# Performance work log

Hardware: AMD Instinct MI355X
Metric: run time of the kernel (lower is better)

The kernel has to match this reference:

```python
import jax, jax.numpy as jnp
import numpy as np

B, S, H, STEPS = 4096, 169, 64, 24  # batch, input seq (window 168 + covariate row), hidden, rollout steps


def _lstm(xseq, Wih, Whh, bih, bhh, h0, c0):
    """PyTorch-style single-layer LSTM. xseq: [B,T,D] -> ([B,T,H], hT, cT). Gate order i,f,g,o."""
    xg = jnp.einsum('btd,gd->btg', xseq, Wih) + (bih + bhh)  # precompute input proj [B,T,4H]

    def step(carry, xg_t):
        h, c = carry
        g = xg_t + h @ Whh.T
        i, f, gg, o = jnp.split(g, 4, axis=-1)
        c = jax.nn.sigmoid(f) * c + jax.nn.sigmoid(i) * jnp.tanh(gg)
        h = jax.nn.sigmoid(o) * jnp.tanh(c)
        return (h, c), h

    (hT, cT), hs = jax.lax.scan(step, (h0, c0), jnp.swapaxes(xg, 0, 1))
    return jnp.swapaxes(hs, 0, 1), hT, cT


def reference(x, Wih1, Whh1, bih1, bhh1, Wih2, Whh2, bih2, bhh2, fc1_w, fc1_b, fc2_w, fc2_b):
    win, d = x[:, :-1, :], x[:, -1, :]  # [B,168,1], [B,1]
    z = jnp.zeros((x.shape[0], H), x.dtype)

    def outer(win, _):
        h1s, h1, c1 = _lstm(win, Wih1, Whh1, bih1, bhh1, z, z)
        h1s = jax.nn.relu(h1s)
        # lstm2 is seeded with lstm1's final (h, c) state, as in the torch code
        h2s, _, _ = _lstm(h1s, Wih2, Whh2, bih2, bhh2, h1, c1)
        feat = jnp.concatenate([jax.nn.relu(h2s[:, -1, :]), d], axis=1)  # [B,65]
        out = (feat @ fc1_w.T + fc1_b) @ fc2_w.T + fc2_b  # [B,1] (no relu between fc1/fc2)
        win = jnp.concatenate([win[:, 1:, :], out[:, :, None]], axis=1)  # slide window
        return win, out[:, 0]

    _, outs = jax.lax.scan(outer, win, None, length=STEPS)  # outs: [24,B]
    return jnp.swapaxes(outs, 0, 1)  # [B,24]


def setup_inputs() -> dict:
    key = jax.random.key(0)
    ks = jax.random.split(key, 14)
    bnd = 1.0 / np.sqrt(H)

    def u(k, shape):
        return jax.random.uniform(k, shape, jnp.float32, -bnd, bnd)

    return {
        'x': jax.random.normal(ks[0], (B, S, 1), jnp.float32),
        'Wih1': u(ks[1], (4 * H, 1)),
        'Whh1': u(ks[2], (4 * H, H)),
        'bih1': u(ks[3], (4 * H,)),
        'bhh1': u(ks[4], (4 * H,)),
        'Wih2': u(ks[5], (4 * H, H)),
        'Whh2': u(ks[6], (4 * H, H)),
        'bih2': u(ks[7], (4 * H,)),
        'bhh2': u(ks[8], (4 * H,)),
        'fc1_w': u(ks[9], (64, 65)),
        'fc1_b': u(ks[10], (64,)),
        'fc2_w': u(ks[11], (1, 64)),
        'fc2_b': u(ks[12], (1,)),
    }
```

## Files before the change

kernel.cpp:

```cpp
#include <hip/hip_runtime.h>
#include <stdint.h>

#define NB 16
#define WIN 168
#define NSTEPS 24
#define NBLK (4096/NB)
#define NT 512

typedef __attribute__((ext_vector_type(8))) short bf16x8;
typedef __attribute__((ext_vector_type(4))) float f32x4;

#if __has_builtin(__builtin_amdgcn_rcpf)
#define RCPF(x) __builtin_amdgcn_rcpf(x)
#else
#define RCPF(x) (1.0f / (x))
#endif
#if __has_builtin(__builtin_amdgcn_exp2f)
#define EXP2F(x) __builtin_amdgcn_exp2f(x)
#else
#define EXP2F(x) __expf((x) * 0.6931471805599453f)
#endif

__device__ __forceinline__ float sigm(float x){
  return RCPF(1.0f + EXP2F(x * -1.4426950408889634f));
}
__device__ __forceinline__ float sigtanh(float a, float b){
  float A = EXP2F(a * -1.4426950408889634f);
  float B = EXP2F(fabsf(b) * -2.8853900817779268f);
  float t = (1.0f - B) * RCPF((1.0f + A) * (1.0f + B));
  uint32_t sb = __builtin_bit_cast(uint32_t, b) & 0x80000000u;
  return __builtin_bit_cast(float, __builtin_bit_cast(uint32_t, t) ^ sb);
}

__device__ __forceinline__ uint32_t bf_rn(float f){
  uint32_t u = __builtin_bit_cast(uint32_t, f);
  return (u + 0x7FFFu + ((u >> 16) & 1u)) >> 16;
}
__device__ __forceinline__ float bf_f(uint32_t s){
  return __builtin_bit_cast(float, s << 16);
}
__device__ __forceinline__ void split_t(float f, uint32_t& hi, uint32_t& lo){
  uint32_t u = __builtin_bit_cast(uint32_t, f);
  hi = u >> 16;
  lo = bf_rn(f - bf_f(hi));
}
__device__ __forceinline__ void split_s(float f, short& hi, short& lo){
  uint32_t h = bf_rn(f);
  hi = (short)h;
  lo = (short)bf_rn(f - bf_f(h));
}
__device__ __forceinline__ f32x4 mfma16(bf16x8 a, bf16x8 b, f32x4 c){
  return __builtin_amdgcn_mfma_f32_16x16x32_bf16(a, b, c, 0, 0, 0);
}

__device__ __forceinline__ void lstm_epi(const f32x4 acc[4], float c[4], float hn[4]){
  #pragma unroll
  for (int r = 0; r < 4; r++){
    float cn = __builtin_fmaf(sigm(acc[1][r]), c[r], sigtanh(acc[0][r], acc[2][r]));
    c[r] = cn;
    hn[r] = sigtanh(acc[3][r], cn);
  }
}

#define FROW 136
#define FBLK 544
#define FB(buf,hl,kt) ((((buf)*2 + (hl))*2 + (kt)) * FBLK)
#define BUF_INTS (2*FBLK)

__global__ __launch_bounds__(NT, 2) void lstm_fused_kernel(
  const float* __restrict__ x,    const float* __restrict__ Wih1, const float* __restrict__ Whh1,
  const float* __restrict__ bih1, const float* __restrict__ bhh1,
  const float* __restrict__ Wih2, const float* __restrict__ Whh2,
  const float* __restrict__ bih2, const float* __restrict__ bhh2,
  const float* __restrict__ fc1w, const float* __restrict__ fc1b,
  const float* __restrict__ fc2w, const float* __restrict__ fc2b,
  float* __restrict__ out, short* __restrict__ hist)
{
  __shared__ __align__(16) short aS[2*2*2*FBLK];
  __shared__ __align__(16) short bS[2*2*2*FBLK];
  __shared__ float cS[64][16];
  __shared__ float win_s[WIN][NB];
  __shared__ float Hlast[NB][68];
  __shared__ float fc1w_s[64*68];
  __shared__ float dval_s[NB];

  const int tid = threadIdx.x;
  const int wv8 = tid >> 6;
  const int wv  = wv8 & 3;
  const bool isA = (wv8 < 4);
  const int ln  = tid & 63;
  const int q   = ln >> 4;
  const int n   = ln & 15;
  const int bg0 = blockIdx.x * NB;
  const int u0  = 16*wv + 4*q;
  const int kt_  = u0 >> 5;
  const int q2_  = (u0 >> 3) & 3;
  const int jj0_ = u0 & 7;
  const int rdo  = q*FROW + n*8;
  const int wro  = q2_*FROW + n*8 + jj0_;
  const int gwo  = kt_*512 + q2_*128 + n*8 + jj0_;
  const int ro   = q*128 + n*8;
  short* __restrict__ hblk = hist + (size_t)blockIdx.x * WIN * 2048;

  for (int i = tid; i < WIN*NB; i += NT){ int t = i >> 4, b = i & 15; win_s[t][b] = x[(bg0 + b)*169 + t]; }
  for (int i = tid; i < 64*65; i += NT){ int j = i / 65, k = i % 65; fc1w_s[j*68 + k] = fc1w[i]; }
  if (tid < NB) dval_s[tid] = x[(bg0 + tid)*169 + 168];

  const float fc1b_r = fc1b[ln];
  const float fc2w_r = fc2w[ln];
  const float fc2b_r = fc2b[0];

  auto fc_head = [&](int s){
    float o2[2];
    #pragma unroll
    for (int bi = 0; bi < 2; bi++){
      const int b = 2*wv8 + bi;
      float a1 = fc1b_r;
      #pragma unroll
      for (int k4 = 0; k4 < 16; k4++){
        const float* wp = &fc1w_s[ln*68 + k4*4];
        const float* hp = &Hlast[b][k4*4];
        a1 += wp[0]*hp[0] + wp[1]*hp[1] + wp[2]*hp[2] + wp[3]*hp[3];
      }
      a1 += dval_s[b] * fc1w_s[ln*68 + 64];
      float v = a1 * fc2w_r;
      #pragma unroll
      for (int off = 32; off > 0; off >>= 1) v += __shfl_xor(v, off);
      o2[bi] = v + fc2b_r;
    }
    if (ln == 0){
      #pragma unroll
      for (int bi = 0; bi < 2; bi++){
        const int b = 2*wv8 + bi;
        out[(bg0 + b)*24 + s] = o2[bi];
        win_s[s % WIN][b] = o2[bi];
      }
    }
  };

  if (isA){
    bf16x8 A1hi[4][2], A1lo[4][2], Ain1[4];
    f32x4 b1c[4];
    #pragma unroll
    for (int e = 0; e < 4; e++){
      const int ja = 64*e + 16*wv + n;
      #pragma unroll
      for (int kt = 0; kt < 2; kt++){
        const float* pw = Whh1 + ja*64 + kt*32 + q*8;
        #pragma unroll
        for (int jj = 0; jj < 8; jj++){ short h,l; split_s(pw[jj], h, l); A1hi[e][kt][jj] = h; A1lo[e][kt][jj] = l; }
      }
      bf16x8 ain = {0,0,0,0,0,0,0,0};
      if (q == 0){ short wh, wl; split_s(Wih1[ja], wh, wl); ain[0] = wh; ain[1] = wh; ain[2] = wl; }
      Ain1[e] = ain;
      const int jc = 64*e + u0;
      #pragma unroll
      for (int r = 0; r < 4; r++) b1c[e][r] = bih1[jc+r] + bhh1[jc+r];
    }
    float c1[4];

    auto lstm1 = [&](int rb, int wb, int slot, int t, bool first){
      f32x4 acc[4];
      bf16x8 bin = {0,0,0,0,0,0,0,0};
      { float xv = win_s[slot][n]; uint32_t xh, xl; split_t(xv, xh, xl);
        if (q == 0){ bin[0] = (short)xh; bin[1] = (short)xl; bin[2] = (short)xh; } }
      if (first){
        #pragma unroll
        for (int e = 0; e < 4; e++) acc[e] = mfma16(Ain1[e], bin, b1c[e]);
      } else {
        bf16x8 Bh0 = *(const bf16x8*)&aS[FB(rb,0,0)+rdo];
        bf16x8 Bl0 = *(const bf16x8*)&aS[FB(rb,1,0)+rdo];
        bf16x8 Bh1 = *(const bf16x8*)&aS[FB(rb,0,1)+rdo];
        bf16x8 Bl1 = *(const bf16x8*)&aS[FB(rb,1,1)+rdo];
        #pragma unroll
        for (int e = 0; e < 4; e++){
          f32x4 a = b1c[e];
          a = mfma16(A1hi[e][0], Bh0, a);
          a = mfma16(A1hi[e][0], Bl0, a);
          a = mfma16(A1lo[e][0], Bh0, a);
          a = mfma16(A1hi[e][1], Bh1, a);
          a = mfma16(A1hi[e][1], Bl1, a);
          a = mfma16(A1lo[e][1], Bh1, a);
          a = mfma16(Ain1[e], bin, a);
          acc[e] = a;
        }
      }
      float hn[4];
      lstm_epi(acc, c1, hn);
      uint32_t ph[4], pl[4];
      #pragma unroll
      for (int r = 0; r < 4; r++) split_t(hn[r], ph[r], pl[r]);
      *(uint2*)&aS[FB(wb,0,kt_)+wro] = make_uint2(ph[0] | (ph[1]<<16), ph[2] | (ph[3]<<16));
      *(uint2*)&aS[FB(wb,1,kt_)+wro] = make_uint2(pl[0] | (pl[1]<<16), pl[2] | (pl[3]<<16));
      uint32_t sh[4], sl[4];
      #pragma unroll
      for (int r = 0; r < 4; r++){ bool pos = hn[r] > 0.0f; sh[r] = pos ? ph[r] : 0u; sl[r] = pos ? pl[r] : 0u; }
      short* Hp = hblk + (size_t)t * 2048;
      *(uint2*)&Hp[gwo]        = make_uint2(sh[0] | (sh[1]<<16), sh[2] | (sh[3]<<16));
      *(uint2*)&Hp[1024 + gwo] = make_uint2(sl[0] | (sl[1]<<16), sl[2] | (sl[3]<<16));
    };

    #pragma unroll
    for (int r = 0; r < 4; r++) c1[r] = 0.0f;
    for (int t = 0; t < WIN; t++){
      __syncthreads();
      lstm1(t & 1, (t & 1) ^ 1, t, t, t == 0);
    }
    #pragma unroll
    for (int r = 0; r < 4; r++) cS[u0 + r][n] = c1[r];

    for (int sg = 1; sg < NSTEPS; sg++){
      #pragma unroll
      for (int r = 0; r < 4; r++) c1[r] = 0.0f;
      int slot = sg;
      __syncthreads();
      lstm1(0, 1, slot, 0, true);
      slot++;
      for (int t = 1; t < WIN-1; t++){
        __syncthreads();
        lstm1(t & 1, (t & 1) ^ 1, slot, t, false);
        slot++; if (slot == WIN) slot = 0;
      }
      __syncthreads();
      __syncthreads();
      fc_head(sg - 1);
      __syncthreads();
      lstm1(1, 0, slot, WIN-1, false);
      #pragma unroll
      for (int r = 0; r < 4; r++) cS[u0 + r][n] = c1[r];
    }

    for (int i = 0; i < WIN + 1; i++) __syncthreads();
    fc_head(NSTEPS - 1);

  } else {
    bf16x8 A2hi[4][4], A2lo[4][4];
    f32x4 b2c[4];
    #pragma unroll
    for (int e = 0; e < 4; e++){
      const int ja = 64*e + 16*wv + n;
      #pragma unroll
      for (int kt = 0; kt < 4; kt++){
        const float* pw = (kt < 2 ? (Wih2 + ja*64 + kt*32) : (Whh2 + ja*64 + (kt-2)*32)) + q*8;
        #pragma unroll
        for (int jj = 0; jj < 8; jj++){ short h,l; split_s(pw[jj], h, l); A2hi[e][kt][jj] = h; A2lo[e][kt][jj] = l; }
      }
      const int jc = 64*e + u0;
      #pragma unroll
      for (int r = 0; r < 4; r++) b2c[e][r] = bih2[jc+r] + bhh2[jc+r];
    }
    float c2[4];
    bf16x8 ch0, cl0, ch1, cl1, nh0, nl0, nh1, nl1;

    auto loadc = [&](int t){
      const short* Hp = hblk + (size_t)t * 2048;
      ch0 = *(const bf16x8*)&Hp[ro];
      cl0 = *(const bf16x8*)&Hp[1024 + ro];
      ch1 = *(const bf16x8*)&Hp[512 + ro];
      cl1 = *(const bf16x8*)&Hp[1536 + ro];
    };
    auto loadn = [&](int t){
      const short* Hp = hblk + (size_t)t * 2048;
      nh0 = *(const bf16x8*)&Hp[ro];
      nl0 = *(const bf16x8*)&Hp[1024 + ro];
      nh1 = *(const bf16x8*)&Hp[512 + ro];
      nl1 = *(const bf16x8*)&Hp[1536 + ro];
    };
    auto shift = [&](){ ch0 = nh0; cl0 = nl0; ch1 = nh1; cl1 = nl1; };

    auto lstm2 = [&](const short* Sr, int rb, short* Sw, int wb, bool last){
      bf16x8 L2h0 = *(const bf16x8*)&Sr[FB(rb,0,0)+rdo];
      bf16x8 L2l0 = *(const bf16x8*)&Sr[FB(rb,1,0)+rdo];
      bf16x8 L2h1 = *(const bf16x8*)&Sr[FB(rb,0,1)+rdo];
      bf16x8 L2l1 = *(const bf16x8*)&Sr[FB(rb,1,1)+rdo];
      f32x4 acc[4];
      #pragma unroll
      for (int e = 0; e < 4; e++){
        f32x4 a = b2c[e];
        a = mfma16(A2hi[e][0], ch0, a);
        a = mfma16(A2hi[e][0], cl0, a);
        a = mfma16(A2lo[e][0], ch0, a);
        a = mfma16(A2hi[e][1], ch1, a);
        a = mfma16(A2hi[e][1], cl1, a);
        a = mfma16(A2lo[e][1], ch1, a);
        a = mfma16(A2hi[e][2], L2h0, a);
        a = mfma16(A2hi[e][2], L2l0, a);
        a = mfma16(A2lo[e][2], L2h0, a);
        a = mfma16(A2hi[e][3], L2h1, a);
        a = mfma16(A2hi[e][3], L2l1, a);
        a = mfma16(A2lo[e][3], L2h1, a);
        acc[e] = a;
      }
      float hn[4];
      lstm_epi(acc, c2, hn);
      if (!last){
        uint32_t ph[4], pl[4];
        #pragma unroll
        for (int r = 0; r < 4; r++) split_t(hn[r], ph[r], pl[r]);
        *(uint2*)&Sw[FB(wb,0,kt_)+wro] = make_uint2(ph[0] | (ph[1]<<16), ph[2] | (ph[3]<<16));
        *(uint2*)&Sw[FB(wb,1,kt_)+wro] = make_uint2(pl[0] | (pl[1]<<16), pl[2] | (pl[3]<<16));
      } else {
        #pragma unroll
        for (int r = 0; r < 4; r++) Hlast[n][u0 + r] = fmaxf(hn[r], 0.0f);
      }
    };

    for (int i = 0; i < WIN; i++) __syncthreads();

    for (int sg = 1; sg < NSTEPS; sg++){
      loadc(0);
      loadn(1);
      __syncthreads();
      #pragma unroll
      for (int r = 0; r < 4; r++) c2[r] = cS[u0 + r][n];
      lstm2(aS, 0, bS, 1, false);
      shift();
      for (int t = 1; t < WIN-1; t++){
        __syncthreads();
        loadn(t + 1);
        lstm2(bS, t & 1, bS, (t & 1) ^ 1, false);
        shift();
      }
      __syncthreads();
      lstm2(bS, 1, bS, 0, true);
      __syncthreads();
      fc_head(sg - 1);
      __syncthreads();
    }

    {
      loadc(0);
      loadn(1);
      __syncthreads();
      #pragma unroll
      for (int r = 0; r < 4; r++) c2[r] = cS[u0 + r][n];
      lstm2(aS, 0, bS, 1, false);
      shift();
      for (int t = 1; t < WIN-1; t++){
        __syncthreads();
        loadn(t + 1);
        lstm2(bS, t & 1, bS, (t & 1) ^ 1, false);
        shift();
      }
      __syncthreads();
      lstm2(bS, 1, bS, 0, true);
      __syncthreads();
      fc_head(NSTEPS - 1);
    }
  }
}

__global__ __launch_bounds__(256, 1) void lstm_fallback_kernel(
  const float* __restrict__ x,    const float* __restrict__ Wih1, const float* __restrict__ Whh1,
  const float* __restrict__ bih1, const float* __restrict__ bhh1,
  const float* __restrict__ Wih2, const float* __restrict__ Whh2,
  const float* __restrict__ bih2, const float* __restrict__ bhh2,
  const float* __restrict__ fc1w, const float* __restrict__ fc1b,
  const float* __restrict__ fc2w, const float* __restrict__ fc2b,
  float* __restrict__ out)
{
  __shared__ __align__(16) short aS[2*2*2*FBLK];
  __shared__ __align__(16) short r1f[2*2*2*FBLK];
  __shared__ __align__(16) short rlf[2*2*2*FBLK];
  __shared__ float win_s[WIN][NB];
  __shared__ float Hlast[NB][68];
  __shared__ float fc1w_s[64*68];
  __shared__ float dval_s[NB];

  const int tid = threadIdx.x;
  const int wv  = tid >> 6;
  const int ln  = tid & 63;
  const int q   = ln >> 4;
  const int n   = ln & 15;
  const int bg0 = blockIdx.x * NB;
  const int u0  = 16*wv + 4*q;
  const int kt_  = u0 >> 5;
  const int q2_  = (u0 >> 3) & 3;
  const int jj0_ = u0 & 7;
  const int rdo  = q*FROW + n*8;
  const int wro  = q2_*FROW + n*8 + jj0_;

  for (int i = tid; i < WIN*NB; i += 256){ int t = i >> 4, b = i & 15; win_s[t][b] = x[(bg0 + b)*169 + t]; }
  for (int i = tid; i < 64*65; i += 256){ int j = i / 65, k = i % 65; fc1w_s[j*68 + k] = fc1w[i]; }
  if (tid < NB) dval_s[tid] = x[(bg0 + tid)*169 + 168];

  const float fc1b_r = fc1b[ln];
  const float fc2w_r = fc2w[ln];
  const float fc2b_r = fc2b[0];

  bf16x8 A1hi[4][2], A1lo[4][2], Ain1[4];
  bf16x8 A2hi[4][4], A2lo[4][4];
  f32x4 b1c[4], b2c[4];
  #pragma unroll
  for (int e = 0; e < 4; e++){
    const int ja = 64*e + 16*wv + n;
    #pragma unroll
    for (int kt = 0; kt < 2; kt++){
      const float* pw = Whh1 + ja*64 + kt*32 + q*8;
      #pragma unroll
      for (int jj = 0; jj < 8; jj++){ short h,l; split_s(pw[jj], h, l); A1hi[e][kt][jj] = h; A1lo[e][kt][jj] = l; }
    }
    #pragma unroll
    for (int kt = 0; kt < 4; kt++){
      const float* pw = (kt < 2 ? (Wih2 + ja*64 + kt*32) : (Whh2 + ja*64 + (kt-2)*32)) + q*8;
      #pragma unroll
      for (int jj = 0; jj < 8; jj++){ short h,l; split_s(pw[jj], h, l); A2hi[e][kt][jj] = h; A2lo[e][kt][jj] = l; }
    }
    bf16x8 ain = {0,0,0,0,0,0,0,0};
    if (q == 0){ short wh, wl; split_s(Wih1[ja], wh, wl); ain[0] = wh; ain[1] = wh; ain[2] = wl; }
    Ain1[e] = ain;
    const int jc = 64*e + u0;
    #pragma unroll
    for (int r = 0; r < 4; r++){
      b1c[e][r] = bih1[jc+r] + bhh1[jc+r];
      b2c[e][r] = bih2[jc+r] + bhh2[jc+r];
    }
  }

  float c1[4], c2[4], c1r[4];

  auto lstm1_step = [&](short* S, float* cst, int rb, int wb, int slot, bool relu_out){
    bf16x8 Bh0 = *(const bf16x8*)&S[FB(rb,0,0)+rdo];
    bf16x8 Bl0 = *(const bf16x8*)&S[FB(rb,1,0)+rdo];
    bf16x8 Bh1 = *(const bf16x8*)&S[FB(rb,0,1)+rdo];
    bf16x8 Bl1 = *(const bf16x8*)&S[FB(rb,1,1)+rdo];
    bf16x8 bin = {0,0,0,0,0,0,0,0};
    { float xv = win_s[slot][n]; uint32_t xh, xl; split_t(xv, xh, xl);
      if (q == 0){ bin[0] = (short)xh; bin[1] = (short)xl; bin[2] = (short)xh; } }
    f32x4 acc[4];
    #pragma unroll
    for (int e = 0; e < 4; e++){
      f32x4 a = b1c[e];
      a = mfma16(A1hi[e][0], Bh0, a);
      a = mfma16(A1hi[e][0], Bl0, a);
      a = mfma16(A1lo[e][0], Bh0, a);
      a = mfma16(A1hi[e][1], Bh1, a);
      a = mfma16(A1hi[e][1], Bl1, a);
      a = mfma16(A1lo[e][1], Bh1, a);
      a = mfma16(Ain1[e], bin, a);
      acc[e] = a;
    }
    float hn[4];
    lstm_epi(acc, cst, hn);
    uint32_t ph[4], pl[4];
    #pragma unroll
    for (int r = 0; r < 4; r++) split_t(hn[r], ph[r], pl[r]);
    *(uint2*)&S[FB(wb,0,kt_)+wro] = make_uint2(ph[0] | (ph[1]<<16), ph[2] | (ph[3]<<16));
    *(uint2*)&S[FB(wb,1,kt_)+wro] = make_uint2(pl[0] | (pl[1]<<16), pl[2] | (pl[3]<<16));
    if (relu_out){
      uint32_t sh[4], sl[4];
      #pragma unroll
      for (int r = 0; r < 4; r++){ bool pos = hn[r] > 0.0f; sh[r] = pos ? ph[r] : 0u; sl[r] = pos ? pl[r] : 0u; }
      *(uint2*)&rlf[FB(rb,0,kt_)+wro] = make_uint2(sh[0] | (sh[1]<<16), sh[2] | (sh[3]<<16));
      *(uint2*)&rlf[FB(rb,1,kt_)+wro] = make_uint2(sl[0] | (sl[1]<<16), sl[2] | (sl[3]<<16));
    }
  };

  auto lstm2_core = [&](bf16x8 L1h0, bf16x8 L1l0, bf16x8 L1h1, bf16x8 L1l1,
                        int rbuf, int wbuf, bool last){
    bf16x8 L2h0 = *(const bf16x8*)&aS[FB(rbuf,0,0)+rdo];
    bf16x8 L2l0 = *(const bf16x8*)&aS[FB(rbuf,1,0)+rdo];
    bf16x8 L2h1 = *(const bf16x8*)&aS[FB(rbuf,0,1)+rdo];
    bf16x8 L2l1 = *(const bf16x8*)&aS[FB(rbuf,1,1)+rdo];
    f32x4 acc[4];
    #pragma unroll
    for (int e = 0; e < 4; e++){
      f32x4 a = b2c[e];
      a = mfma16(A2hi[e][0], L1h0, a);
      a = mfma16(A2hi[e][0], L1l0, a);
      a = mfma16(A2lo[e][0], L1h0, a);
      a = mfma16(A2hi[e][1], L1h1, a);
      a = mfma16(A2hi[e][1], L1l1, a);
      a = mfma16(A2lo[e][1], L1h1, a);
      a = mfma16(A2hi[e][2], L2h0, a);
      a = mfma16(A2hi[e][2], L2l0, a);
      a = mfma16(A2lo[e][2], L2h0, a);
      a = mfma16(A2hi[e][3], L2h1, a);
      a = mfma16(A2hi[e][3], L2l1, a);
      a = mfma16(A2lo[e][3], L2h1, a);
      acc[e] = a;
    }
    float hn[4];
    lstm_epi(acc, c2, hn);
    if (!last){
      uint32_t ph[4], pl[4];
      #pragma unroll
      for (int r = 0; r < 4; r++) split_t(hn[r], ph[r], pl[r]);
      *(uint2*)&aS[FB(wbuf,0,kt_)+wro] = make_uint2(ph[0] | (ph[1]<<16), ph[2] | (ph[3]<<16));
      *(uint2*)&aS[FB(wbuf,1,kt_)+wro] = make_uint2(pl[0] | (pl[1]<<16), pl[2] | (pl[3]<<16));
    } else {
      #pragma unroll
      for (int r = 0; r < 4; r++) Hlast[n][u0 + r] = fmaxf(hn[r], 0.0f);
    }
  };

  for (int s = 0; s < NSTEPS; s++){
    { int* p = (int*)&aS[0];
      for (int i = tid; i < BUF_INTS; i += 256) p[i] = 0; }
    #pragma unroll
    for (int r = 0; r < 4; r++) c1[r] = 0.0f;
    int slot = s;
    for (int t = 0; t < WIN; t++){
      __syncthreads();
      lstm1_step(aS, c1, t & 1, (t & 1) ^ 1, slot, false);
      slot++; if (slot == WIN) slot = 0;
    }
    #pragma unroll
    for (int r = 0; r < 4; r++){ c2[r] = c1[r]; c1r[r] = 0.0f; }
    { int* p = (int*)&r1f[0];
      for (int i = tid; i < BUF_INTS; i += 256) p[i] = 0; }
    slot = s;
    __syncthreads();
    lstm1_step(r1f, c1r, 0, 1, slot, true);
    slot++;
    for (int i = 1; i < WIN; i++){
      __syncthreads();
      const int rb = i & 1, wb = rb ^ 1;
      lstm1_step(r1f, c1r, rb, wb, slot, true);
      bf16x8 L1h0 = *(const bf16x8*)&rlf[FB(wb,0,0)+rdo];
      bf16x8 L1l0 = *(const bf16x8*)&rlf[FB(wb,1,0)+rdo];
      bf16x8 L1h1 = *(const bf16x8*)&rlf[FB(wb,0,1)+rdo];
      bf16x8 L1l1 = *(const bf16x8*)&rlf[FB(wb,1,1)+rdo];
      lstm2_core(L1h0, L1l0, L1h1, L1l1, wb, rb, false);
      slot++; if (slot == WIN) slot = 0;
    }
    __syncthreads();
    {
      const int rb = (WIN - 1) & 1;
      bf16x8 L1h0 = *(const bf16x8*)&rlf[FB(rb,0,0)+rdo];
      bf16x8 L1l0 = *(const bf16x8*)&rlf[FB(rb,1,0)+rdo];
      bf16x8 L1h1 = *(const bf16x8*)&rlf[FB(rb,0,1)+rdo];
      bf16x8 L1l1 = *(const bf16x8*)&rlf[FB(rb,1,1)+rdo];
      lstm2_core(L1h0, L1l0, L1h1, L1l1, rb, 0, true);
    }
    __syncthreads();
    {
      float o4[4];
      #pragma unroll
      for (int bi = 0; bi < 4; bi++){
        const int b = 4*wv + bi;
        float a1 = fc1b_r;
        #pragma unroll
        for (int k4 = 0; k4 < 16; k4++){
          const float* wp = &fc1w_s[ln*68 + k4*4];
          const float* hp = &Hlast[b][k4*4];
          a1 += wp[0]*hp[0] + wp[1]*hp[1] + wp[2]*hp[2] + wp[3]*hp[3];
        }
        a1 += dval_s[b] * fc1w_s[ln*68 + 64];
        float v = a1 * fc2w_r;
        #pragma unroll
        for (int off = 32; off > 0; off >>= 1) v += __shfl_xor(v, off);
        o4[bi] = v + fc2b_r;
      }
      if (ln == 0){
        #pragma unroll
        for (int bi = 0; bi < 4; bi++){
          const int b = 4*wv + bi;
          out[(bg0 + b)*24 + s] = o4[bi];
          win_s[s % WIN][b] = o4[bi];
        }
      }
    }
  }
}

extern "C" void kernel_launch(void* const* d_in, const int* in_sizes, int n_in,
                              void* d_out, int out_size, void* d_ws, size_t ws_size,
                              hipStream_t stream) {
  (void)in_sizes; (void)n_in; (void)out_size;
  const size_t need = (size_t)NBLK * WIN * 2048 * sizeof(short);
  if (ws_size >= need){
    lstm_fused_kernel<<<dim3(NBLK), dim3(NT), 0, stream>>>(
        (const float*)d_in[0], (const float*)d_in[1], (const float*)d_in[2],
        (const float*)d_in[3], (const float*)d_in[4], (const float*)d_in[5],
        (const float*)d_in[6], (const float*)d_in[7], (const float*)d_in[8],
        (const float*)d_in[9], (const float*)d_in[10], (const float*)d_in[11],
        (const float*)d_in[12], (float*)d_out, (short*)d_ws);
  } else {
    lstm_fallback_kernel<<<dim3(NBLK), dim3(256), 0, stream>>>(
        (const float*)d_in[0], (const float*)d_in[1], (const float*)d_in[2],
        (const float*)d_in[3], (const float*)d_in[4], (const float*)d_in[5],
        (const float*)d_in[6], (const float*)d_in[7], (const float*)d_in[8],
        (const float*)d_in[9], (const float*)d_in[10], (const float*)d_in[11],
        (const float*)d_in[12], (float*)d_out);
  }
}
```

Measured before the change: 4.958 ms.

## Replace block-wide barriers with LDS counter flags between LSTM1 and LSTM2 warp groups

Replaces the per-timestep __syncthreads between the LSTM1 and LSTM2 wave groups with LDS atomic counters and spin-waits, so each group waits only on the progress it actually depends on. The FC head moves entirely into the LSTM2 waves. The aim is to let the two layers run in a looser pipeline and drop full-block barrier stalls. It adds spin-wait polling, relies on volatile LDS reads and manual waitcnt fences for memory ordering, and carries a risk of subtle races or hangs.

Result: slower. 5.931 ms (+19.6%).

```diff
diff --git a/kernel.cpp b/kernel.cpp
--- a/kernel.cpp
+++ b/kernel.cpp
@@ -5,7 +5,6 @@
 #define WIN 168
 #define NSTEPS 24
 #define NBLK (4096/NB)
-#define NT 512
 
 typedef __attribute__((ext_vector_type(8))) short bf16x8;
 typedef __attribute__((ext_vector_type(4))) float f32x4;
@@ -67,7 +66,11 @@
 #define FB(buf,hl,kt) ((((buf)*2 + (hl))*2 + (kt)) * FBLK)
 #define BUF_INTS (2*FBLK)
 
-__global__ __launch_bounds__(NT, 2) void lstm_fused_kernel(
+#define LGKM_FENCE() __asm__ volatile("s_waitcnt lgkmcnt(0)" ::: "memory")
+#define VM_FENCE()   __asm__ volatile("s_waitcnt vmcnt(0)" ::: "memory")
+#define CC_FENCE()   __asm__ volatile("" ::: "memory")
+
+__global__ __launch_bounds__(512, 2) void lstm_decoupled_kernel(
   const float* __restrict__ x,    const float* __restrict__ Wih1, const float* __restrict__ Whh1,
   const float* __restrict__ bih1, const float* __restrict__ bhh1,
   const float* __restrict__ Wih2, const float* __restrict__ Whh2,
@@ -83,6 +86,7 @@
   __shared__ float Hlast[NB][68];
   __shared__ float fc1w_s[64*68];
   __shared__ float dval_s[NB];
+  __shared__ int barA, barB;
 
   const int tid = threadIdx.x;
   const int wv8 = tid >> 6;
@@ -102,41 +106,19 @@
   const int ro   = q*128 + n*8;
   short* __restrict__ hblk = hist + (size_t)blockIdx.x * WIN * 2048;
 
-  for (int i = tid; i < WIN*NB; i += NT){ int t = i >> 4, b = i & 15; win_s[t][b] = x[(bg0 + b)*169 + t]; }
-  for (int i = tid; i < 64*65; i += NT){ int j = i / 65, k = i % 65; fc1w_s[j*68 + k] = fc1w[i]; }
+  for (int i = tid; i < WIN*NB; i += 512){ int t = i >> 4, b = i & 15; win_s[t][b] = x[(bg0 + b)*169 + t]; }
+  for (int i = tid; i < 64*65; i += 512){ int j = i / 65, k = i % 65; fc1w_s[j*68 + k] = fc1w[i]; }
   if (tid < NB) dval_s[tid] = x[(bg0 + tid)*169 + 168];
+  if (tid == 0){ barA = 0; barB = 0; }
 
   const float fc1b_r = fc1b[ln];
   const float fc2w_r = fc2w[ln];
   const float fc2b_r = fc2b[0];
 
-  auto fc_head = [&](int s){
-    float o2[2];
-    #pragma unroll
-    for (int bi = 0; bi < 2; bi++){
-      const int b = 2*wv8 + bi;
-      float a1 = fc1b_r;
-      #pragma unroll
-      for (int k4 = 0; k4 < 16; k4++){
-        const float* wp = &fc1w_s[ln*68 + k4*4];
-        const float* hp = &Hlast[b][k4*4];
-        a1 += wp[0]*hp[0] + wp[1]*hp[1] + wp[2]*hp[2] + wp[3]*hp[3];
-      }
-      a1 += dval_s[b] * fc1w_s[ln*68 + 64];
-      float v = a1 * fc2w_r;
-      #pragma unroll
-      for (int off = 32; off > 0; off >>= 1) v += __shfl_xor(v, off);
-      o2[bi] = v + fc2b_r;
-    }
-    if (ln == 0){
-      #pragma unroll
-      for (int bi = 0; bi < 2; bi++){
-        const int b = 2*wv8 + bi;
-        out[(bg0 + b)*24 + s] = o2[bi];
-        win_s[s % WIN][b] = o2[bi];
-      }
-    }
-  };
+  __syncthreads();
+
+  volatile int* vA = &barA;
+  volatile int* vB = &barB;
 
   if (isA){
     bf16x8 A1hi[4][2], A1lo[4][2], Ain1[4];
@@ -158,80 +140,73 @@
       for (int r = 0; r < 4; r++) b1c[e][r] = bih1[jc+r] + bhh1[jc+r];
     }
     float c1[4];
-
-    auto lstm1 = [&](int rb, int wb, int slot, int t, bool first){
-      f32x4 acc[4];
-      bf16x8 bin = {0,0,0,0,0,0,0,0};
-      { float xv = win_s[slot][n]; uint32_t xh, xl; split_t(xv, xh, xl);
-        if (q == 0){ bin[0] = (short)xh; bin[1] = (short)xl; bin[2] = (short)xh; } }
-      if (first){
-        #pragma unroll
-        for (int e = 0; e < 4; e++) acc[e] = mfma16(Ain1[e], bin, b1c[e]);
-      } else {
-        bf16x8 Bh0 = *(const bf16x8*)&aS[FB(rb,0,0)+rdo];
-        bf16x8 Bl0 = *(const bf16x8*)&aS[FB(rb,1,0)+rdo];
-        bf16x8 Bh1 = *(const bf16x8*)&aS[FB(rb,0,1)+rdo];
-        bf16x8 Bl1 = *(const bf16x8*)&aS[FB(rb,1,1)+rdo];
-        #pragma unroll
-        for (int e = 0; e < 4; e++){
-          f32x4 a = b1c[e];
-          a = mfma16(A1hi[e][0], Bh0, a);
-          a = mfma16(A1hi[e][0], Bl0, a);
-          a = mfma16(A1lo[e][0], Bh0, a);
-          a = mfma16(A1hi[e][1], Bh1, a);
-          a = mfma16(A1hi[e][1], Bl1, a);
-          a = mfma16(A1lo[e][1], Bh1, a);
-          a = mfma16(Ain1[e], bin, a);
-          acc[e] = a;
-        }
-      }
-      float hn[4];
-      lstm_epi(acc, c1, hn);
-      uint32_t ph[4], pl[4];
-      #pragma unroll
-      for (int r = 0; r < 4; r++) split_t(hn[r], ph[r], pl[r]);
-      *(uint2*)&aS[FB(wb,0,kt_)+wro] = make_uint2(ph[0] | (ph[1]<<16), ph[2] | (ph[3]<<16));
-      *(uint2*)&aS[FB(wb,1,kt_)+wro] = make_uint2(pl[0] | (pl[1]<<16), pl[2] | (pl[3]<<16));
-      uint32_t sh[4], sl[4];
-      #pragma unroll
-      for (int r = 0; r < 4; r++){ bool pos = hn[r] > 0.0f; sh[r] = pos ? ph[r] : 0u; sl[r] = pos ? pl[r] : 0u; }
-      short* Hp = hblk + (size_t)t * 2048;
-      *(uint2*)&Hp[gwo]        = make_uint2(sh[0] | (sh[1]<<16), sh[2] | (sh[3]<<16));
-      *(uint2*)&Hp[1024 + gwo] = make_uint2(sl[0] | (sl[1]<<16), sl[2] | (sl[3]<<16));
-    };
-
-    #pragma unroll
-    for (int r = 0; r < 4; r++) c1[r] = 0.0f;
-    for (int t = 0; t < WIN; t++){
-      __syncthreads();
-      lstm1(t & 1, (t & 1) ^ 1, t, t, t == 0);
-    }
-    #pragma unroll
-    for (int r = 0; r < 4; r++) cS[u0 + r][n] = c1[r];
-
-    for (int sg = 1; sg < NSTEPS; sg++){
+    int gA = 0;
+
+    for (int sg = 0; sg < NSTEPS; sg++){
       #pragma unroll
       for (int r = 0; r < 4; r++) c1[r] = 0.0f;
       int slot = sg;
-      __syncthreads();
-      lstm1(0, 1, slot, 0, true);
-      slot++;
-      for (int t = 1; t < WIN-1; t++){
-        __syncthreads();
-        lstm1(t & 1, (t & 1) ^ 1, slot, t, false);
+      for (int t = 0; t < WIN; t++){
+        int tb = 0;
+        if (sg > 0) tb = (t == WIN-1) ? 4*169*sg : 4*((sg-1)*169 + t + 1);
+        if (ln == 0){
+          const int ta = 4*gA;
+          while (*vA < ta) {}
+          while (*vB < tb) {}
+        }
+        CC_FENCE();
+        {
+          const int rb = t & 1, wb = rb ^ 1;
+          f32x4 acc[4];
+          bf16x8 bin = {0,0,0,0,0,0,0,0};
+          { float xv = win_s[slot][n]; uint32_t xh, xl; split_t(xv, xh, xl);
+            if (q == 0){ bin[0] = (short)xh; bin[1] = (short)xl; bin[2] = (short)xh; } }
+          if (t == 0){
+            #pragma unroll
+            for (int e = 0; e < 4; e++) acc[e] = mfma16(Ain1[e], bin, b1c[e]);
+          } else {
+            bf16x8 Bh0 = *(const bf16x8*)&aS[FB(rb,0,0)+rdo];
+            bf16x8 Bl0 = *(const bf16x8*)&aS[FB(rb,1,0)+rdo];
+            bf16x8 Bh1 = *(const bf16x8*)&aS[FB(rb,0,1)+rdo];
+            bf16x8 Bl1 = *(const bf16x8*)&aS[FB(rb,1,1)+rdo];
+            #pragma unroll
+            for (int e = 0; e < 4; e++){
+              f32x4 a = b1c[e];
+              a = mfma16(A1hi[e][0], Bh0, a);
+              a = mfma16(A1hi[e][0], Bl0, a);
+              a = mfma16(A1lo[e][0], Bh0, a);
+              a = mfma16(A1hi[e][1], Bh1, a);
+              a = mfma16(A1hi[e][1], Bl1, a);
+              a = mfma16(A1lo[e][1], Bh1, a);
+              a = mfma16(Ain1[e], bin, a);
+              acc[e] = a;
+            }
+          }
+          float hn[4];
+          lstm_epi(acc, c1, hn);
+          uint32_t ph[4], pl[4];
+          #pragma unroll
+          for (int r = 0; r < 4; r++) split_t(hn[r], ph[r], pl[r]);
+          *(uint2*)&aS[FB(wb,0,kt_)+wro] = make_uint2(ph[0] | (ph[1]<<16), ph[2] | (ph[3]<<16));
+          *(uint2*)&aS[FB(wb,1,kt_)+wro] = make_uint2(pl[0] | (pl[1]<<16), pl[2] | (pl[3]<<16));
+          uint32_t sh[4], sl[4];
+          #pragma unroll
+          for (int r = 0; r < 4; r++){ bool pos = hn[r] > 0.0f; sh[r] = pos ? ph[r] : 0u; sl[r] = pos ? pl[r] : 0u; }
+          short* Hp = hblk + (size_t)t * 2048;
+          *(uint2*)&Hp[gwo]        = make_uint2(sh[0] | (sh[1]<<16), sh[2] | (sh[3]<<16));
+          *(uint2*)&Hp[1024 + gwo] = make_uint2(sl[0] | (sl[1]<<16), sl[2] | (sl[3]<<16));
+          if (t == WIN-1){
+            #pragma unroll
+            for (int r = 0; r < 4; r++) cS[u0 + r][n] = c1[r];
+          }
+        }
+        LGKM_FENCE();
+        if (t == WIN-1) VM_FENCE();
+        if (ln == 0) atomicAdd(&barA, 1);
+        gA++;
         slot++; if (slot == WIN) slot = 0;
       }
-      __syncthreads();
-      __syncthreads();
-      fc_head(sg - 1);
-      __syncthreads();
-      lstm1(1, 0, slot, WIN-1, false);
-      #pragma unroll
-      for (int r = 0; r < 4; r++) cS[u0 + r][n] = c1[r];
-    }
-
-    for (int i = 0; i < WIN + 1; i++) __syncthreads();
-    fc_head(NSTEPS - 1);
+    }
 
   } else {
     bf16x8 A2hi[4][4], A2lo[4][4];
@@ -251,14 +226,8 @@
     }
     float c2[4];
     bf16x8 ch0, cl0, ch1, cl1, nh0, nl0, nh1, nl1;
-
-    auto loadc = [&](int t){
-      const short* Hp = hblk + (size_t)t * 2048;
-      ch0 = *(const bf16x8*)&Hp[ro];
-      cl0 = *(const bf16x8*)&Hp[1024 + ro];
-      ch1 = *(const bf16x8*)&Hp[512 + ro];
-      cl1 = *(const bf16x8*)&Hp[1536 + ro];
-    };
+    int gB = 0;
+
     auto loadn = [&](int t){
       const short* Hp = hblk + (size_t)t * 2048;
       nh0 = *(const bf16x8*)&Hp[ro];
@@ -266,86 +235,104 @@
       nh1 = *(const bf16x8*)&Hp[512 + ro];
       nl1 = *(const bf16x8*)&Hp[1536 + ro];
     };
-    auto shift = [&](){ ch0 = nh0; cl0 = nl0; ch1 = nh1; cl1 = nl1; };
-
-    auto lstm2 = [&](const short* Sr, int rb, short* Sw, int wb, bool last){
-      bf16x8 L2h0 = *(const bf16x8*)&Sr[FB(rb,0,0)+rdo];
-      bf16x8 L2l0 = *(const bf16x8*)&Sr[FB(rb,1,0)+rdo];
-      bf16x8 L2h1 = *(const bf16x8*)&Sr[FB(rb,0,1)+rdo];
-      bf16x8 L2l1 = *(const bf16x8*)&Sr[FB(rb,1,1)+rdo];
-      f32x4 acc[4];
-      #pragma unroll
-      for (int e = 0; e < 4; e++){
-        f32x4 a = b2c[e];
-        a = mfma16(A2hi[e][0], ch0, a);
-        a = mfma16(A2hi[e][0], cl0, a);
-        a = mfma16(A2lo[e][0], ch0, a);
-        a = mfma16(A2hi[e][1], ch1, a);
-        a = mfma16(A2hi[e][1], cl1, a);
-        a = mfma16(A2lo[e][1], ch1, a);
-        a = mfma16(A2hi[e][2], L2h0, a);
-        a = mfma16(A2hi[e][2], L2l0, a);
-        a = mfma16(A2lo[e][2], L2h0, a);
-        a = mfma16(A2hi[e][3], L2h1, a);
-        a = mfma16(A2hi[e][3], L2l1, a);
-        a = mfma16(A2lo[e][3], L2h1, a);
-        acc[e] = a;
-      }
-      float hn[4];
-      lstm_epi(acc, c2, hn);
-      if (!last){
-        uint32_t ph[4], pl[4];
+
+    for (int sb = 0; sb < NSTEPS; sb++){
+      for (int t = 0; t < WIN; t++){
+        if (ln == 0){
+          const int tb = 4*gB;
+          while (*vB < tb) {}
+          if (t == 0){ const int ta = 4*168*(sb+1); while (*vA < ta) {} }
+        }
+        CC_FENCE();
+        if (t == 0){
+          #pragma unroll
+          for (int r = 0; r < 4; r++) c2[r] = cS[u0 + r][n];
+          const short* Hp = hblk;
+          ch0 = *(const bf16x8*)&Hp[ro];
+          cl0 = *(const bf16x8*)&Hp[1024 + ro];
+          ch1 = *(const bf16x8*)&Hp[512 + ro];
+          cl1 = *(const bf16x8*)&Hp[1536 + ro];
+          loadn(1);
+        } else if (t < WIN-1){
+          loadn(t + 1);
+        }
+        {
+          const bool last = (t == WIN-1);
+          const short* Sr = (t == 0) ? aS : bS;
+          const int rb = (t == 0) ? 0 : (t & 1);
+          const int wb = (t == 0) ? 1 : ((t & 1) ^ 1);
+          bf16x8 L2h0 = *(const bf16x8*)&Sr[FB(rb,0,0)+rdo];
+          bf16x8 L2l0 = *(const bf16x8*)&Sr[FB(rb,1,0)+rdo];
+          bf16x8 L2h1 = *(const bf16x8*)&Sr[FB(rb,0,1)+rdo];
+          bf16x8 L2l1 = *(const bf16x8*)&Sr[FB(rb,1,1)+rdo];
+          f32x4 acc[4];
+          #pragma unroll
+          for (int e = 0; e < 4; e++){
+            f32x4 a = b2c[e];
+            a = mfma16(A2hi[e][0], ch0, a);
+            a = mfma16(A2hi[e][0], cl0, a);
+            a = mfma16(A2lo[e][0], ch0, a);
+            a = mfma16(A2hi[e][1], ch1, a);
+            a = mfma16(A2hi[e][1], cl1, a);
+            a = mfma16(A2lo[e][1], ch1, a);
+            a = mfma16(A2hi[e][2], L2h0, a);
+            a = mfma16(A2hi[e][2], L2l0, a);
+            a = mfma16(A2lo[e][2], L2h0, a);
+            a = mfma16(A2hi[e][3], L2h1, a);
+            a = mfma16(A2hi[e][3], L2l1, a);
+            a = mfma16(A2lo[e][3], L2h1, a);
+            acc[e] = a;
+          }
+          float hn[4];
+          lstm_epi(acc, c2, hn);
+          if (!last){
+            uint32_t ph[4], pl[4];
+            #pragma unroll
+            for (int r = 0; r < 4; r++) split_t(hn[r], ph[r], pl[r]);
+            *(uint2*)&bS[FB(wb,0,kt_)+wro] = make_uint2(ph[0] | (ph[1]<<16), ph[2] | (ph[3]<<16));
+            *(uint2*)&bS[FB(wb,1,kt_)+wro] = make_uint2(pl[0] | (pl[1]<<16), pl[2] | (pl[3]<<16));
+          } else {
+            #pragma unroll
+            for (int r = 0; r < 4; r++) Hlast[n][u0 + r] = fmaxf(hn[r], 0.0f);
+          }
+          ch0 = nh0; cl0 = nl0; ch1 = nh1; cl1 = nl1;
+        }
+        LGKM_FENCE();
+        if (ln == 0) atomicAdd(&barB, 1);
+        gB++;
+      }
+      if (ln == 0){ const int tb = 4*gB; while (*vB < tb) {} }
+      CC_FENCE();
+      {
+        float o4[4];
         #pragma unroll
-        for (int r = 0; r < 4; r++) split_t(hn[r], ph[r], pl[r]);
-        *(uint2*)&Sw[FB(wb,0,kt_)+wro] = make_uint2(ph[0] | (ph[1]<<16), ph[2] | (ph[3]<<16));
-        *(uint2*)&Sw[FB(wb,1,kt_)+wro] = make_uint2(pl[0] | (pl[1]<<16), pl[2] | (pl[3]<<16));
-      } else {
-        #pragma unroll
-        for (int r = 0; r < 4; r++) Hlast[n][u0 + r] = fmaxf(hn[r], 0.0f);
-      }
-    };
-
-    for (int i = 0; i < WIN; i++) __syncthreads();
-
-    for (int sg = 1; sg < NSTEPS; sg++){
-      loadc(0);
-      loadn(1);
-      __syncthreads();
-      #pragma unroll
-      for (int r = 0; r < 4; r++) c2[r] = cS[u0 + r][n];
-      lstm2(aS, 0, bS, 1, false);
-      shift();
-      for (int t = 1; t < WIN-1; t++){
-        __syncthreads();
-        loadn(t + 1);
-        lstm2(bS, t & 1, bS, (t & 1) ^ 1, false);
-        shift();
-      }
-      __syncthreads();
-      lstm2(bS, 1, bS, 0, true);
-      __syncthreads();
-      fc_head(sg - 1);
-      __syncthreads();
-    }
-
-    {
-      loadc(0);
-      loadn(1);
-      __syncthreads();
-      #pragma unroll
-      for (int r = 0; r < 4; r++) c2[r] = cS[u0 + r][n];
-      lstm2(aS, 0, bS, 1, false);
-      shift();
-      for (int t = 1; t < WIN-1; t++){
-        __syncthreads();
-        loadn(t + 1);
-        lstm2(bS, t & 1, bS, (t & 1) ^ 1, false);
-        shift();
-      }
-      __syncthreads();
-      lstm2(bS, 1, bS, 0, true);
-      __syncthreads();
-      fc_head(NSTEPS - 1);
+        for (int bi = 0; bi < 4; bi++){
+          const int b = 4*wv + bi;
+          float a1 = fc1b_r;
+          #pragma unroll
+          for (int k4 = 0; k4 < 16; k4++){
+            const float* wp = &fc1w_s[ln*68 + k4*4];
+            const float* hp = &Hlast[b][k4*4];
+            a1 += wp[0]*hp[0] + wp[1]*hp[1] + wp[2]*hp[2] + wp[3]*hp[3];
+          }
+          a1 += dval_s[b] * fc1w_s[ln*68 + 64];
+          float v = a1 * fc2w_r;
+          #pragma unroll
+          for (int off = 32; off > 0; off >>= 1) v += __shfl_xor(v, off);
+          o4[bi] = v + fc2b_r;
+        }
+        if (ln == 0){
+          #pragma unroll
+          for (int bi = 0; bi < 4; bi++){
+            const int b = 4*wv + bi;
+            out[(bg0 + b)*24 + sb] = o4[bi];
+            win_s[sb][b] = o4[bi];
+          }
+        }
+      }
+      LGKM_FENCE();
+      if (ln == 0) atomicAdd(&barB, 1);
+      gB++;
     }
   }
 }
@@ -570,7 +557,7 @@
   (void)in_sizes; (void)n_in; (void)out_size;
   const size_t need = (size_t)NBLK * WIN * 2048 * sizeof(short);
   if (ws_size >= need){
-    lstm_fused_kernel<<<dim3(NBLK), dim3(NT), 0, stream>>>(
+    lstm_decoupled_kernel<<<dim3(NBLK), dim3(512), 0, stream>>>(
         (const float*)d_in[0], (const float*)d_in[1], (const float*)d_in[2],
         (const float*)d_in[3], (const float*)d_in[4], (const float*)d_in[5],
         (const float*)d_in[6], (const float*)d_in[7], (const float*)d_in[8],
```

## Move LSTM2 input projection to LSTM1 warps via shared-memory partial sums

Applied to the files above, without the earlier changes.

The input-projection half of LSTM2's gate GEMM (Wih2·relu(h1)) moves from the LSTM2 warps to the LSTM1 warps. The LSTM1 warps now load the h1 history and compute that partial, then write it to a double-buffered shared array. LSTM2 warps start from these partials, so each of their steps runs only the recurrent Whh2 half, halving MFMA work on the LSTM2 critical path. In exchange the LSTM1 warps carry more registers and MFMA work, and shared-memory use grows by about 32 KB, which may limit the two-blocks-per-CU occupancy.

New measurement: 5.224 ms. 5.4% more time.

```diff
diff --git a/kernel.cpp b/kernel.cpp
--- a/kernel.cpp
+++ b/kernel.cpp
@@ -66,6 +66,10 @@
 #define FBLK 544
 #define FB(buf,hl,kt) ((((buf)*2 + (hl))*2 + (kt)) * FBLK)
 #define BUF_INTS (2*FBLK)
+
+#define PS_E   256
+#define PS_WV  (4*PS_E)
+#define PS_PB  (4*PS_WV)
 
 __global__ __launch_bounds__(NT, 2) void lstm_fused_kernel(
   const float* __restrict__ x,    const float* __restrict__ Wih1, const float* __restrict__ Whh1,
@@ -78,6 +82,7 @@
 {
   __shared__ __align__(16) short aS[2*2*2*FBLK];
   __shared__ __align__(16) short bS[2*2*2*FBLK];
+  __shared__ __align__(16) float pS[2*PS_PB];
   __shared__ float cS[64][16];
   __shared__ float win_s[WIN][NB];
   __shared__ float Hlast[NB][68];
@@ -100,6 +105,7 @@
   const int wro  = q2_*FROW + n*8 + jj0_;
   const int gwo  = kt_*512 + q2_*128 + n*8 + jj0_;
   const int ro   = q*128 + n*8;
+  const int pso  = wv*PS_WV + q*64 + n*4;
   short* __restrict__ hblk = hist + (size_t)blockIdx.x * WIN * 2048;
 
   for (int i = tid; i < WIN*NB; i += NT){ int t = i >> 4, b = i & 15; win_s[t][b] = x[(bg0 + b)*169 + t]; }
@@ -140,7 +146,8 @@
 
   if (isA){
     bf16x8 A1hi[4][2], A1lo[4][2], Ain1[4];
-    f32x4 b1c[4];
+    bf16x8 A2hi[4][2], A2lo[4][2];
+    f32x4 b1c[4], b2c[4];
     #pragma unroll
     for (int e = 0; e < 4; e++){
       const int ja = 64*e + 16*wv + n;
@@ -149,15 +156,46 @@
         const float* pw = Whh1 + ja*64 + kt*32 + q*8;
         #pragma unroll
         for (int jj = 0; jj < 8; jj++){ short h,l; split_s(pw[jj], h, l); A1hi[e][kt][jj] = h; A1lo[e][kt][jj] = l; }
+      }
+      #pragma unroll
+      for (int kt = 0; kt < 2; kt++){
+        const float* pw = Wih2 + ja*64 + kt*32 + q*8;
+        #pragma unroll
+        for (int jj = 0; jj < 8; jj++){ short h,l; split_s(pw[jj], h, l); A2hi[e][kt][jj] = h; A2lo[e][kt][jj] = l; }
       }
       bf16x8 ain = {0,0,0,0,0,0,0,0};
       if (q == 0){ short wh, wl; split_s(Wih1[ja], wh, wl); ain[0] = wh; ain[1] = wh; ain[2] = wl; }
       Ain1[e] = ain;
       const int jc = 64*e + u0;
       #pragma unroll
-      for (int r = 0; r < 4; r++) b1c[e][r] = bih1[jc+r] + bhh1[jc+r];
+      for (int r = 0; r < 4; r++){
+        b1c[e][r] = bih1[jc+r] + bhh1[jc+r];
+        b2c[e][r] = bih2[jc+r] + bhh2[jc+r];
+      }
     }
     float c1[4];
+    bf16x8 rh0, rl0, rh1, rl1;
+
+    auto hloadA = [&](int t){
+      const short* Hp = hblk + (size_t)t * 2048;
+      rh0 = *(const bf16x8*)&Hp[ro];
+      rl0 = *(const bf16x8*)&Hp[1024 + ro];
+      rh1 = *(const bf16x8*)&Hp[512 + ro];
+      rl1 = *(const bf16x8*)&Hp[1536 + ro];
+    };
+    auto partial2 = [&](int pb){
+      #pragma unroll
+      for (int e = 0; e < 4; e++){
+        f32x4 a = b2c[e];
+        a = mfma16(A2hi[e][0], rh0, a);
+        a = mfma16(A2hi[e][0], rl0, a);
+        a = mfma16(A2lo[e][0], rh0, a);
+        a = mfma16(A2hi[e][1], rh1, a);
+        a = mfma16(A2hi[e][1], rl1, a);
+        a = mfma16(A2lo[e][1], rh1, a);
+        *(f32x4*)&pS[pb*PS_PB + pso + e*PS_E] = a;
+      }
+    };
 
     auto lstm1 = [&](int rb, int wb, int slot, int t, bool first){
       f32x4 acc[4];
@@ -202,10 +240,14 @@
 
     #pragma unroll
     for (int r = 0; r < 4; r++) c1[r] = 0.0f;
-    for (int t = 0; t < WIN; t++){
+    for (int t = 0; t < WIN-1; t++){
       __syncthreads();
       lstm1(t & 1, (t & 1) ^ 1, t, t, t == 0);
     }
+    __syncthreads();
+    hloadA(0);
+    lstm1(1, 0, WIN-1, WIN-1, false);
+    partial2(0);
     #pragma unroll
     for (int r = 0; r < 4; r++) cS[u0 + r][n] = c1[r];
 
@@ -214,81 +256,68 @@
       for (int r = 0; r < 4; r++) c1[r] = 0.0f;
       int slot = sg;
       __syncthreads();
+      hloadA(1);
       lstm1(0, 1, slot, 0, true);
+      partial2(1);
       slot++;
       for (int t = 1; t < WIN-1; t++){
         __syncthreads();
+        hloadA(t + 1);
         lstm1(t & 1, (t & 1) ^ 1, slot, t, false);
+        partial2((t + 1) & 1);
         slot++; if (slot == WIN) slot = 0;
       }
       __syncthreads();
+      hloadA(0);
       __syncthreads();
       fc_head(sg - 1);
       __syncthreads();
       lstm1(1, 0, slot, WIN-1, false);
+      partial2(0);
       #pragma unroll
       for (int r = 0; r < 4; r++) cS[u0 + r][n] = c1[r];
     }
 
-    for (int i = 0; i < WIN + 1; i++) __syncthreads();
+    for (int i = 0; i < WIN-1; i++){
+      __syncthreads();
+      hloadA(i + 1);
+      partial2((i + 1) & 1);
+    }
+    __syncthreads();
+    __syncthreads();
     fc_head(NSTEPS - 1);
 
   } else {
-    bf16x8 A2hi[4][4], A2lo[4][4];
-    f32x4 b2c[4];
+    bf16x8 B2hi[4][2], B2lo[4][2];
     #pragma unroll
     for (int e = 0; e < 4; e++){
       const int ja = 64*e + 16*wv + n;
       #pragma unroll
-      for (int kt = 0; kt < 4; kt++){
-        const float* pw = (kt < 2 ? (Wih2 + ja*64 + kt*32) : (Whh2 + ja*64 + (kt-2)*32)) + q*8;
-        #pragma unroll
-        for (int jj = 0; jj < 8; jj++){ short h,l; split_s(pw[jj], h, l); A2hi[e][kt][jj] = h; A2lo[e][kt][jj] = l; }
-      }
-      const int jc = 64*e + u0;
-      #pragma unroll
-      for (int r = 0; r < 4; r++) b2c[e][r] = bih2[jc+r] + bhh2[jc+r];
+      for (int kt = 0; kt < 2; kt++){
+        const float* pw = Whh2 + ja*64 + kt*32 + q*8;
+        #pragma unroll
+        for (int jj = 0; jj < 8; jj++){ short h,l; split_s(pw[jj], h, l); B2hi[e][kt][jj] = h; B2lo[e][kt][jj] = l; }
+      }
     }
     float c2[4];
-    bf16x8 ch0, cl0, ch1, cl1, nh0, nl0, nh1, nl1;
-
-    auto loadc = [&](int t){
-      const short* Hp = hblk + (size_t)t * 2048;
-      ch0 = *(const bf16x8*)&Hp[ro];
-      cl0 = *(const bf16x8*)&Hp[1024 + ro];
-      ch1 = *(const bf16x8*)&Hp[512 + ro];
-      cl1 = *(const bf16x8*)&Hp[1536 + ro];
-    };
-    auto loadn = [&](int t){
-      const short* Hp = hblk + (size_t)t * 2048;
-      nh0 = *(const bf16x8*)&Hp[ro];
-      nl0 = *(const bf16x8*)&Hp[1024 + ro];
-      nh1 = *(const bf16x8*)&Hp[512 + ro];
-      nl1 = *(const bf16x8*)&Hp[1536 + ro];
-    };
-    auto shift = [&](){ ch0 = nh0; cl0 = nl0; ch1 = nh1; cl1 = nl1; };
-
-    auto lstm2 = [&](const short* Sr, int rb, short* Sw, int wb, bool last){
+
+    auto lstm2 = [&](const short* Sr, int rb, short* Sw, int wb, int pb, bool last){
+      f32x4 acc[4];
+      #pragma unroll
+      for (int e = 0; e < 4; e++) acc[e] = *(const f32x4*)&pS[pb*PS_PB + pso + e*PS_E];
       bf16x8 L2h0 = *(const bf16x8*)&Sr[FB(rb,0,0)+rdo];
       bf16x8 L2l0 = *(const bf16x8*)&Sr[FB(rb,1,0)+rdo];
       bf16x8 L2h1 = *(const bf16x8*)&Sr[FB(rb,0,1)+rdo];
       bf16x8 L2l1 = *(const bf16x8*)&Sr[FB(rb,1,1)+rdo];
-      f32x4 acc[4];
       #pragma unroll
       for (int e = 0; e < 4; e++){
-        f32x4 a = b2c[e];
-        a = mfma16(A2hi[e][0], ch0, a);
-        a = mfma16(A2hi[e][0], cl0, a);
-        a = mfma16(A2lo[e][0], ch0, a);
-        a = mfma16(A2hi[e][1], ch1, a);
-        a = mfma16(A2hi[e][1], cl1, a);
-        a = mfma16(A2lo[e][1], ch1, a);
-        a = mfma16(A2hi[e][2], L2h0, a);
-        a = mfma16(A2hi[e][2], L2l0, a);
-        a = mfma16(A2lo[e][2], L2h0, a);
-        a = mfma16(A2hi[e][3], L2h1, a);
-        a = mfma16(A2hi[e][3], L2l1, a);
-        a = mfma16(A2lo[e][3], L2h1, a);
+        f32x4 a = acc[e];
+        a = mfma16(B2hi[e][0], L2h0, a);
+        a = mfma16(B2hi[e][0], L2l0, a);
+        a = mfma16(B2lo[e][0], L2h0, a);
+        a = mfma16(B2hi[e][1], L2h1, a);
+        a = mfma16(B2hi[e][1], L2l1, a);
+        a = mfma16(B2lo[e][1], L2h1, a);
         acc[e] = a;
       }
       float hn[4];
@@ -308,42 +337,32 @@
     for (int i = 0; i < WIN; i++) __syncthreads();
 
     for (int sg = 1; sg < NSTEPS; sg++){
-      loadc(0);
-      loadn(1);
       __syncthreads();
       #pragma unroll
       for (int r = 0; r < 4; r++) c2[r] = cS[u0 + r][n];
-      lstm2(aS, 0, bS, 1, false);
-      shift();
+      lstm2(aS, 0, bS, 1, 0, false);
       for (int t = 1; t < WIN-1; t++){
         __syncthreads();
-        loadn(t + 1);
-        lstm2(bS, t & 1, bS, (t & 1) ^ 1, false);
-        shift();
-      }
-      __syncthreads();
-      lstm2(bS, 1, bS, 0, true);
+        lstm2(bS, t & 1, bS, (t & 1) ^ 1, t & 1, false);
+      }
+      __syncthreads();
+      lstm2(bS, 1, bS, 0, 1, true);
       __syncthreads();
       fc_head(sg - 1);
       __syncthreads();
     }
 
     {
-      loadc(0);
-      loadn(1);
       __syncthreads();
       #pragma unroll
       for (int r = 0; r < 4; r++) c2[r] = cS[u0 + r][n];
-      lstm2(aS, 0, bS, 1, false);
-      shift();
+      lstm2(aS, 0, bS, 1, 0, false);
       for (int t = 1; t < WIN-1; t++){
         __syncthreads();
-        loadn(t + 1);
-        lstm2(bS, t & 1, bS, (t & 1) ^ 1, false);
-        shift();
-      }
-      __syncthreads();
-      lstm2(bS, 1, bS, 0, true);
+        lstm2(bS, t & 1, bS, (t & 1) ^ 1, t & 1, false);
+      }
+      __syncthreads();
+      lstm2(bS, 1, bS, 0, 1, true);
       __syncthreads();
       fc_head(NSTEPS - 1);
     }
```
